# Kernel optimization log

Hardware: AMD Instinct MI355X
Metric: run time of the kernel (lower is better)

## Reference

```python
import jax, jax.numpy as jnp
import numpy as np

B, C, D = 16384, 4096, 512
ALPHA = 0.1
BETA = 0.25


def setup_inputs() -> dict:
    key = jax.random.key(0)
    kx, kc = jax.random.split(key)
    x = jax.random.normal(kx, (B, D), dtype=jnp.float32)
    codes = jax.random.normal(kc, (1, C, D), dtype=jnp.float32)
    return {"x": x, "codes": codes}


def reference(x, codes):
    # x: (B, D), codes: (1, C, D). Eval-mode forward of Quantizer (l2 metric).
    d = x.shape[1]
    c = codes[0]                                  # (C, D)
    # squared l2 distance via expansion (same math as sum((x-c)^2, -1))
    x_sq = jnp.sum(x * x, axis=-1, keepdims=True)  # (B, 1)
    c_sq = jnp.sum(c * c, axis=-1)                 # (C,)
    dots = jnp.einsum('bd,cd->bc', x, c)           # (B, C)
    raw_distances = x_sq + c_sq[None, :] - 2.0 * dots
    distances = raw_distances / d / ALPHA          # scaling preserved for faithfulness
    indices = jnp.argmin(distances, axis=-1)       # (B,)
    quantized = c[indices]                         # (B, D) gather
    # commit loss: dist(x, stop_grad(quantized)); codebook loss: dist(stop_grad(x), quantized)
    diff_commit = x - jax.lax.stop_gradient(quantized)
    loss_commit = jnp.mean(jnp.sum(diff_commit * diff_commit, axis=-1))
    diff_code = jax.lax.stop_gradient(x) - quantized
    loss_codebook = jnp.mean(jnp.sum(diff_code * diff_code, axis=-1))
    loss = loss_commit + BETA * loss_codebook
    return quantized, indices, loss
```

## Files before the change

### kernel.cpp

```cpp
#include <hip/hip_runtime.h>

#define B_SZ 16384
#define C_SZ 4096
#define D_SZ 512

#define QSCALE 22.7f
#define INV_S2 (1.0f / (QSCALE * QSCALE))
#define EPS 6.0f
#define DBIAS 1024.0f

typedef __attribute__((ext_vector_type(4))) int intx4;

__device__ inline unsigned q4(const float4 v) {
    int a = (int)rintf(v.x * QSCALE); a = max(-127, min(127, a));
    int b = (int)rintf(v.y * QSCALE); b = max(-127, min(127, b));
    int c = (int)rintf(v.z * QSCALE); c = max(-127, min(127, c));
    int d = (int)rintf(v.w * QSCALE); d = max(-127, min(127, d));
    return ((unsigned)(a & 255)) | ((unsigned)(b & 255) << 8) |
           ((unsigned)(c & 255) << 16) | ((unsigned)(d & 255) << 24);
}
__device__ inline void gload16(const void* g, void* l) {
    __builtin_amdgcn_global_load_lds(
        (const __attribute__((address_space(1))) void*)g,
        (__attribute__((address_space(3))) void*)l, 16, 0, 0);
}

__global__ __launch_bounds__(256) void convert_kernel(const float* __restrict__ x,
                                                      const float* __restrict__ codes,
                                                      unsigned* __restrict__ xq,
                                                      unsigned* __restrict__ cq,
                                                      float* __restrict__ csq) {
    const int XB = (B_SZ * D_SZ) / 4 / 256;
    if (blockIdx.x < XB) {
        const int tid = blockIdx.x * 256 + threadIdx.x;
        const float4 v = ((const float4*)x)[tid];
        xq[tid] = q4(v);
    } else {
        const int t = threadIdx.x;
        const int wave = t >> 6;
        const int lane = t & 63;
        const int code = (blockIdx.x - XB) * 4 + wave;
        const float4* cp = (const float4*)(codes + (size_t)code * D_SZ);
        float s = 0.0f;
        #pragma unroll
        for (int u = 0; u < 2; ++u) {
            const float4 v = cp[lane + 64 * u];
            cq[(size_t)code * (D_SZ / 4) + lane + 64 * u] = q4(v);
            s = fmaf(v.x, v.x, s); s = fmaf(v.y, v.y, s);
            s = fmaf(v.z, v.z, s); s = fmaf(v.w, v.w, s);
        }
        #pragma unroll
        for (int off = 32; off; off >>= 1) s += __shfl_down(s, off, 64);
        if (lane == 0) csq[code] = s;
    }
}

__global__ __launch_bounds__(512, 6) void gemm_argmin_kernel(
        const unsigned char* __restrict__ xq,
        const unsigned char* __restrict__ cq,
        const float* __restrict__ csq,
        uint2* __restrict__ table) {
    __shared__ unsigned char sA[128][128];
    __shared__ unsigned char sB[128][128];

    const int t = threadIdx.x;
    const int wave = t >> 6;
    const int lane = t & 63;
    const int quad = lane >> 4;
    const int l15 = lane & 15;

    const int rowbase = blockIdx.y * 128;
    const int colbase = blockIdx.x * 128;
    const int wr = (wave >> 1) * 32;
    const int wc = (wave & 1) * 64;

    const unsigned char* gsrc;
    unsigned char(*ltile)[128];
    int rowoff;
    if (wave < 4) { gsrc = xq ? xq + (size_t)rowbase * D_SZ : xq; ltile = sA; rowoff = wave * 32; }
    else          { gsrc = cq + (size_t)colbase * D_SZ; ltile = sB; rowoff = (wave - 4) * 32; }
    const int lrow = lane >> 3;
    const int lchunk = (lane & 7) ^ (lrow & 7);
    const unsigned char* gbase = gsrc + (size_t)(rowoff + lrow) * D_SZ + lchunk * 16;

    float cs2[4];
    #pragma unroll
    for (int j = 0; j < 4; ++j)
        cs2[j] = fmaf(0.5f, csq[colbase + wc + j * 16 + l15], DBIAS);

    intx4 acc[2][4];
    #pragma unroll
    for (int i = 0; i < 2; ++i)
        #pragma unroll
        for (int j = 0; j < 4; ++j) acc[i][j] = (intx4)0;

    for (int kt = 0; kt < D_SZ / 128; ++kt) {
        const unsigned char* g = gbase + kt * 128;
        #pragma unroll
        for (int inst = 0; inst < 4; ++inst)
            gload16(g + (size_t)(inst * 8) * D_SZ, &ltile[rowoff + inst * 8][0]);
        __syncthreads();

        #pragma unroll
        for (int ksub = 0; ksub < 2; ++ksub) {
            const int cc = (((ksub * 4 + quad) ^ (l15 & 7))) * 16;
            intx4 a[2], b[4];
            #pragma unroll
            for (int i = 0; i < 2; ++i)
                a[i] = *(const intx4*)&sA[wr + i * 16 + l15][cc];
            #pragma unroll
            for (int j = 0; j < 4; ++j)
                b[j] = *(const intx4*)&sB[wc + j * 16 + l15][cc];
            #pragma unroll
            for (int i = 0; i < 2; ++i)
                #pragma unroll
                for (int j = 0; j < 4; ++j)
                    acc[i][j] = __builtin_amdgcn_mfma_i32_16x16x64_i8(a[i], b[j], acc[i][j], 0, 0, 0);
        }
        __syncthreads();
    }

    const int hb = blockIdx.x * 2 + (wave & 1);

    #pragma unroll
    for (int i = 0; i < 2; ++i) {
        #pragma unroll
        for (int r = 0; r < 4; ++r) {
            unsigned k[4];
            #pragma unroll
            for (int j = 0; j < 4; ++j) {
                const float d = fmaf(-(float)acc[i][j][r], INV_S2, cs2[j]);
                k[j] = (__float_as_uint(d) & 0xFFFFFFC0u) | (unsigned)(j * 16 + l15);
            }
            const unsigned lo1 = min(k[0], k[1]), hi1 = max(k[0], k[1]);
            const unsigned lo2 = min(k[2], k[3]), hi2 = max(k[2], k[3]);
            unsigned k1 = min(lo1, lo2);
            unsigned k2 = min(max(lo1, lo2), min(hi1, hi2));
            #pragma unroll
            for (int off = 8; off; off >>= 1) {
                const unsigned ok1 = (unsigned)__shfl_down((int)k1, off, 16);
                const unsigned ok2 = (unsigned)__shfl_down((int)k2, off, 16);
                const unsigned hi = max(k1, ok1);
                const unsigned w2 = (k1 < ok1) ? k2 : ok2;
                k1 = min(k1, ok1);
                k2 = min(hi, w2);
            }
            if (l15 == 0) {
                const int grow = rowbase + wr + i * 16 + quad * 4 + r;
                table[(size_t)grow * 64 + hb] = make_uint2(k1, k2);
            }
        }
    }
}

__global__ __launch_bounds__(256) void rerank_gather_loss_kernel(
        const float* __restrict__ x,
        const float* __restrict__ codes,
        const float* __restrict__ csq,
        const uint2* __restrict__ table,
        float* __restrict__ outq,
        float* __restrict__ out_idx_f,
        float* __restrict__ partials) {
    __shared__ float red[4];
    const int t = threadIdx.x;
    const int wave = t >> 6;
    const int lane = t & 63;
    const int row0 = (blockIdx.x * 4 + wave) * 4;

    uint2 e[4];
    float4 xv[4][2];
    #pragma unroll
    for (int r = 0; r < 4; ++r) {
        e[r] = table[(size_t)(row0 + r) * 64 + lane];
        const float4* xp = (const float4*)(x + (size_t)(row0 + r) * D_SZ);
        xv[r][0] = xp[lane];
        xv[r][1] = xp[lane + 64];
    }

    int fin[4];
    #pragma unroll
    for (int r = 0; r < 4; ++r) {
        const unsigned k1 = e[r].x, k2 = e[r].y;
        unsigned mk = k1;
        #pragma unroll
        for (int off = 32; off; off >>= 1)
            mk = min(mk, (unsigned)__shfl_xor((int)mk, off, 64));

        const float thr = __uint_as_float(mk & 0xFFFFFFC0u) + EPS;
        const float v1 = __uint_as_float(k1 & 0xFFFFFFC0u);
        const float v2 = __uint_as_float(k2 & 0xFFFFFFC0u);
        const unsigned long long b1 = __ballot(v1 <= thr);
        const unsigned long long b2 = __ballot(v2 <= thr);

        const unsigned long long bm = __ballot(k1 == mk);
        fin[r] = (__ffsll(bm) - 1) * 64 + (int)(mk & 63u);

        if (__popcll(b1) + __popcll(b2) > 1) {
            const int c1 = lane * 64 + (int)(k1 & 63u);
            const int c2 = lane * 64 + (int)(k2 & 63u);
            float bv = 3.4e38f; int bi = 0x7FFFFFFF;
            #pragma unroll
            for (int pass = 0; pass < 2; ++pass) {
                unsigned long long bb = pass ? b2 : b1;
                const int myc = pass ? c2 : c1;
                while (bb) {
                    const int src = __ffsll((unsigned long long)bb) - 1;
                    bb &= bb - 1;
                    const int ci = __shfl(myc, src, 64);
                    const float4* cp = (const float4*)(codes + (size_t)ci * D_SZ);
                    const float4 c0 = cp[lane];
                    const float4 c1v = cp[lane + 64];
                    float s = 0.0f;
                    s = fmaf(xv[r][0].x, c0.x, s);  s = fmaf(xv[r][0].y, c0.y, s);
                    s = fmaf(xv[r][0].z, c0.z, s);  s = fmaf(xv[r][0].w, c0.w, s);
                    s = fmaf(xv[r][1].x, c1v.x, s); s = fmaf(xv[r][1].y, c1v.y, s);
                    s = fmaf(xv[r][1].z, c1v.z, s); s = fmaf(xv[r][1].w, c1v.w, s);
                    #pragma unroll
                    for (int off = 32; off; off >>= 1) s += __shfl_xor(s, off, 64);
                    const float d = fmaf(0.5f, csq[ci], -s);
                    if (d < bv || (d == bv && ci < bi)) { bv = d; bi = ci; }
                }
            }
            fin[r] = bi;
        }
    }

    float4 qv[4][2];
    #pragma unroll
    for (int r = 0; r < 4; ++r) {
        const float4* qp = (const float4*)(codes + (size_t)fin[r] * D_SZ);
        qv[r][0] = qp[lane];
        qv[r][1] = qp[lane + 64];
    }

    float s = 0.0f;
    #pragma unroll
    for (int r = 0; r < 4; ++r) {
        float4* op = (float4*)(outq + (size_t)(row0 + r) * D_SZ);
        op[lane] = qv[r][0];
        op[lane + 64] = qv[r][1];
        const float d0 = xv[r][0].x - qv[r][0].x, d1 = xv[r][0].y - qv[r][0].y;
        const float d2 = xv[r][0].z - qv[r][0].z, d3 = xv[r][0].w - qv[r][0].w;
        const float d4 = xv[r][1].x - qv[r][1].x, d5 = xv[r][1].y - qv[r][1].y;
        const float d6 = xv[r][1].z - qv[r][1].z, d7 = xv[r][1].w - qv[r][1].w;
        s += d0 * d0 + d1 * d1 + d2 * d2 + d3 * d3 + d4 * d4 + d5 * d5 + d6 * d6 + d7 * d7;
        if (lane == 0) out_idx_f[row0 + r] = (float)fin[r];
    }
    #pragma unroll
    for (int off = 32; off; off >>= 1) s += __shfl_down(s, off, 64);
    if (lane == 0) red[wave] = s;
    __syncthreads();
    if (t == 0) partials[blockIdx.x] = red[0] + red[1] + red[2] + red[3];
}

__global__ __launch_bounds__(256) void loss_reduce_kernel(const float* __restrict__ partials,
                                                          float* __restrict__ loss_slot) {
    __shared__ float red[4];
    const int t = threadIdx.x;
    const int wave = t >> 6;
    const int lane = t & 63;
    float s = 0.0f;
    #pragma unroll
    for (int i = 0; i < (B_SZ / 16) / 256; ++i) s += partials[i * 256 + t];
    #pragma unroll
    for (int off = 32; off; off >>= 1) s += __shfl_down(s, off, 64);
    if (lane == 0) red[wave] = s;
    __syncthreads();
    if (t == 0)
        *loss_slot = (red[0] + red[1] + red[2] + red[3]) * (1.25f / (float)B_SZ);
}

extern "C" void kernel_launch(void* const* d_in, const int* in_sizes, int n_in,
                              void* d_out, int out_size, void* d_ws, size_t ws_size,
                              hipStream_t stream) {
    const float* x = (const float*)d_in[0];
    const float* codes = (const float*)d_in[1];

    float* outq = (float*)d_out;
    float* out_idx_f = outq + (size_t)B_SZ * D_SZ;
    float* loss_slot = out_idx_f + B_SZ;

    unsigned char* xq = (unsigned char*)d_ws;
    unsigned char* cq = xq + (size_t)B_SZ * D_SZ;
    float* csq = (float*)(cq + (size_t)C_SZ * D_SZ);
    uint2* table = (uint2*)(csq + C_SZ);
    float* partials = (float*)(table + (size_t)B_SZ * 64);

    const int XB = (B_SZ * D_SZ) / 4 / 256;
    const int CB = C_SZ / 4;
    convert_kernel<<<XB + CB, 256, 0, stream>>>(x, codes, (unsigned*)xq, (unsigned*)cq, csq);
    gemm_argmin_kernel<<<dim3(C_SZ / 128, B_SZ / 128), 512, 0, stream>>>(xq, cq, csq, table);
    rerank_gather_loss_kernel<<<B_SZ / 16, 256, 0, stream>>>(x, codes, csq, table, outq, out_idx_f, partials);
    loss_reduce_kernel<<<1, 256, 0, stream>>>(partials, loss_slot);
}
```

Before: 164.8 us.

## Widen GEMM block tile to 128x256 with 64x64 per-wave tiles

The int8 GEMM+argmin kernel now covers 256 codes per block instead of 128, and each wave computes a 64x64 output tile (4x4 MFMAs) instead of 32x64. All waves now load both the A and B tiles. This raises arithmetic intensity and halves the reloads of the x tile across column blocks. The cost is more accumulator registers, a larger LDS footprint, and a launch-bounds occupancy hint lowered from 6 to 4. The table layout stays 64 half-blocks per row, so the downstream rerank kernel is unchanged.

```diff
diff --git a/kernel.cpp b/kernel.cpp
--- a/kernel.cpp
+++ b/kernel.cpp
@@ -55,64 +55,63 @@
     }
 }
 
-__global__ __launch_bounds__(512, 6) void gemm_argmin_kernel(
+__global__ __launch_bounds__(512, 4) void gemm_argmin_kernel(
         const unsigned char* __restrict__ xq,
         const unsigned char* __restrict__ cq,
         const float* __restrict__ csq,
         uint2* __restrict__ table) {
     __shared__ unsigned char sA[128][128];
-    __shared__ unsigned char sB[128][128];
+    __shared__ unsigned char sB[256][128];
 
     const int t = threadIdx.x;
     const int wave = t >> 6;
     const int lane = t & 63;
     const int quad = lane >> 4;
     const int l15 = lane & 15;
+    const int wm = wave >> 2;
+    const int wn = wave & 3;
 
     const int rowbase = blockIdx.y * 128;
-    const int colbase = blockIdx.x * 128;
-    const int wr = (wave >> 1) * 32;
-    const int wc = (wave & 1) * 64;
-
-    const unsigned char* gsrc;
-    unsigned char(*ltile)[128];
-    int rowoff;
-    if (wave < 4) { gsrc = xq ? xq + (size_t)rowbase * D_SZ : xq; ltile = sA; rowoff = wave * 32; }
-    else          { gsrc = cq + (size_t)colbase * D_SZ; ltile = sB; rowoff = (wave - 4) * 32; }
+    const int colbase = blockIdx.x * 256;
+
     const int lrow = lane >> 3;
-    const int lchunk = (lane & 7) ^ (lrow & 7);
-    const unsigned char* gbase = gsrc + (size_t)(rowoff + lrow) * D_SZ + lchunk * 16;
+    const int lchunk = (lane & 7) ^ lrow;
+    const unsigned char* gA = xq + (size_t)(rowbase + wave * 16 + lrow) * D_SZ + lchunk * 16;
+    const unsigned char* gB = cq + (size_t)(colbase + wave * 32 + lrow) * D_SZ + lchunk * 16;
 
     float cs2[4];
     #pragma unroll
     for (int j = 0; j < 4; ++j)
-        cs2[j] = fmaf(0.5f, csq[colbase + wc + j * 16 + l15], DBIAS);
-
-    intx4 acc[2][4];
-    #pragma unroll
-    for (int i = 0; i < 2; ++i)
+        cs2[j] = fmaf(0.5f, csq[colbase + wn * 64 + j * 16 + l15], DBIAS);
+
+    intx4 acc[4][4];
+    #pragma unroll
+    for (int i = 0; i < 4; ++i)
         #pragma unroll
         for (int j = 0; j < 4; ++j) acc[i][j] = (intx4)0;
 
     for (int kt = 0; kt < D_SZ / 128; ++kt) {
-        const unsigned char* g = gbase + kt * 128;
-        #pragma unroll
-        for (int inst = 0; inst < 4; ++inst)
-            gload16(g + (size_t)(inst * 8) * D_SZ, &ltile[rowoff + inst * 8][0]);
+        const unsigned char* ga = gA + kt * 128;
+        const unsigned char* gb = gB + kt * 128;
+        gload16(ga,                    &sA[wave * 16][0]);
+        gload16(ga + (size_t)8 * D_SZ, &sA[wave * 16 + 8][0]);
+        #pragma unroll
+        for (int u = 0; u < 4; ++u)
+            gload16(gb + (size_t)(u * 8) * D_SZ, &sB[wave * 32 + u * 8][0]);
         __syncthreads();
 
         #pragma unroll
         for (int ksub = 0; ksub < 2; ++ksub) {
             const int cc = (((ksub * 4 + quad) ^ (l15 & 7))) * 16;
-            intx4 a[2], b[4];
-            #pragma unroll
-            for (int i = 0; i < 2; ++i)
-                a[i] = *(const intx4*)&sA[wr + i * 16 + l15][cc];
+            intx4 a[4], b[4];
+            #pragma unroll
+            for (int i = 0; i < 4; ++i)
+                a[i] = *(const intx4*)&sA[wm * 64 + i * 16 + l15][cc];
             #pragma unroll
             for (int j = 0; j < 4; ++j)
-                b[j] = *(const intx4*)&sB[wc + j * 16 + l15][cc];
-            #pragma unroll
-            for (int i = 0; i < 2; ++i)
+                b[j] = *(const intx4*)&sB[wn * 64 + j * 16 + l15][cc];
+            #pragma unroll
+            for (int i = 0; i < 4; ++i)
                 #pragma unroll
                 for (int j = 0; j < 4; ++j)
                     acc[i][j] = __builtin_amdgcn_mfma_i32_16x16x64_i8(a[i], b[j], acc[i][j], 0, 0, 0);
@@ -120,10 +119,10 @@
         __syncthreads();
     }
 
-    const int hb = blockIdx.x * 2 + (wave & 1);
-
-    #pragma unroll
-    for (int i = 0; i < 2; ++i) {
+    const int hb = blockIdx.x * 4 + wn;
+
+    #pragma unroll
+    for (int i = 0; i < 4; ++i) {
         #pragma unroll
         for (int r = 0; r < 4; ++r) {
             unsigned k[4];
@@ -146,7 +145,7 @@
                 k2 = min(hi, w2);
             }
             if (l15 == 0) {
-                const int grow = rowbase + wr + i * 16 + quad * 4 + r;
+                const int grow = rowbase + wm * 64 + i * 16 + quad * 4 + r;
                 table[(size_t)grow * 64 + hb] = make_uint2(k1, k2);
             }
         }
@@ -289,7 +288,7 @@
     const int XB = (B_SZ * D_SZ) / 4 / 256;
     const int CB = C_SZ / 4;
     convert_kernel<<<XB + CB, 256, 0, stream>>>(x, codes, (unsigned*)xq, (unsigned*)cq, csq);
-    gemm_argmin_kernel<<<dim3(C_SZ / 128, B_SZ / 128), 512, 0, stream>>>(xq, cq, csq, table);
+    gemm_argmin_kernel<<<dim3(C_SZ / 256, B_SZ / 128), 512, 0, stream>>>(xq, cq, csq, table);
     rerank_gather_loss_kernel<<<B_SZ / 16, 256, 0, stream>>>(x, codes, csq, table, outq, out_idx_f, partials);
     loss_reduce_kernel<<<1, 256, 0, stream>>>(partials, loss_slot);
 }
```

Result: no change. 166.5 us (+1.0%).
